# Kernel optimization log

Measured on AMD Instinct MI355X. Metric: run time of the kernel, lower is better.

The kernel has to match this reference:

```python
import jax, jax.numpy as jnp
import numpy as np

B, H, S, D = 1, 16, 4096, 64

def setup_inputs() -> dict:
    key = jax.random.key(0)
    kq, kk, kv = jax.random.split(key, 3)
    q = jax.random.normal(kq, (B, H, S, D), dtype=jnp.float32)
    k = jax.random.normal(kk, (B, H, S, D), dtype=jnp.float32)
    v = jax.random.normal(kv, (B, H, S, D), dtype=jnp.float32)
    return {"q": q, "k": k, "v": v}

def reference(q, k, v):
    # attn = q @ k^T  -> [B,H,S,S]; output = attn @ v -> [B,H,S,D]
    attn = jnp.einsum('bhqd,bhkd->bhqk', q, k)
    out = jnp.einsum('bhqk,bhkd->bhqd', attn, v)
    return out
```

## Files before the change

kernel.cpp:

```cpp
#include <hip/hip_runtime.h>
#include <stddef.h>


#define SLEN 4096
#define DIM  64
#define NH   16
#define CH   32
#define RPC  128

typedef float f4v __attribute__((ext_vector_type(4)));

__global__ __launch_bounds__(256) void kvT_partial(const float* __restrict__ K,
                                                   const float* __restrict__ V,
                                                   float* __restrict__ P) {
    const int c = blockIdx.x, h = blockIdx.y, t = threadIdx.x;
    const int wave = t >> 6, lane = t & 63;
    const int i = lane >> 3, j = lane & 7;

    __shared__ float Ks[64][64];
    __shared__ float Vs[64][64];

    const f4v* K4 = (const f4v*)(K + ((size_t)h * SLEN + (size_t)c * RPC) * DIM);
    const f4v* V4 = (const f4v*)(V + ((size_t)h * SLEN + (size_t)c * RPC) * DIM);

    float acc[8][8];
    #pragma unroll
    for (int a = 0; a < 8; ++a) {
        #pragma unroll
        for (int b = 0; b < 8; ++b) acc[a][b] = 0.f;
    }

    f4v kst[4], vst[4];
    #pragma unroll
    for (int u = 0; u < 4; ++u) { kst[u] = K4[u * 256 + t]; vst[u] = V4[u * 256 + t]; }

    for (int tile = 0; tile < 2; ++tile) {
        __syncthreads();
        #pragma unroll
        for (int u = 0; u < 4; ++u) {
            int idx = u * 256 + t, row = idx >> 4, c4 = idx & 15;
            *(f4v*)&Ks[row][c4 * 4] = kst[u];
            *(f4v*)&Vs[row][c4 * 4] = vst[u];
        }
        __syncthreads();
        if (tile == 0) {
            #pragma unroll
            for (int u = 0; u < 4; ++u) {
                kst[u] = K4[1024 + u * 256 + t];
                vst[u] = V4[1024 + u * 256 + t];
            }
        }
        #pragma unroll
        for (int s0 = 0; s0 < 16; ++s0) {
            const int s = wave * 16 + s0;
            float kf[8], vf[8];
            *(f4v*)&kf[0] = *(const f4v*)&Ks[s][i * 8];
            *(f4v*)&kf[4] = *(const f4v*)&Ks[s][i * 8 + 4];
            *(f4v*)&vf[0] = *(const f4v*)&Vs[s][j * 8];
            *(f4v*)&vf[4] = *(const f4v*)&Vs[s][j * 8 + 4];
            #pragma unroll
            for (int a = 0; a < 8; ++a) {
                #pragma unroll
                for (int b = 0; b < 8; ++b)
                    acc[a][b] = fmaf(kf[a], vf[b], acc[a][b]);
            }
        }
    }

    __syncthreads();
    float* M0 = &Ks[0][0];
    float* M1 = &Vs[0][0];
    if (wave == 0 || wave == 2) {
        float* dst = (wave == 0) ? M0 : M1;
        #pragma unroll
        for (int r = 0; r < 8; ++r) {
            #pragma unroll
            for (int hh = 0; hh < 2; ++hh) {
                f4v x; x[0]=acc[r][hh*4]; x[1]=acc[r][hh*4+1]; x[2]=acc[r][hh*4+2]; x[3]=acc[r][hh*4+3];
                *(f4v*)&dst[(i * 8 + r) * 64 + j * 8 + hh * 4] = x;
            }
        }
    }
    __syncthreads();
    if (wave == 1 || wave == 3) {
        float* dst = (wave == 1) ? M0 : M1;
        #pragma unroll
        for (int r = 0; r < 8; ++r) {
            #pragma unroll
            for (int hh = 0; hh < 2; ++hh) {
                f4v x = *(f4v*)&dst[(i * 8 + r) * 64 + j * 8 + hh * 4];
                x[0]+=acc[r][hh*4]; x[1]+=acc[r][hh*4+1]; x[2]+=acc[r][hh*4+2]; x[3]+=acc[r][hh*4+3];
                *(f4v*)&dst[(i * 8 + r) * 64 + j * 8 + hh * 4] = x;
            }
        }
    }
    __syncthreads();
    float* Pc = P + ((size_t)h * CH + c) * (DIM * DIM);
    #pragma unroll
    for (int u = 0; u < 4; ++u) {
        int idx = u * 256 + t;
        f4v x = ((const f4v*)M0)[idx] + ((const f4v*)M1)[idx];
        ((f4v*)Pc)[idx] = x;
    }
}

__global__ __launch_bounds__(256) void reduceM(const float* __restrict__ P,
                                               float* __restrict__ M) {
    const int q = blockIdx.x, h = blockIdx.y, t = threadIdx.x;
    const int off = q * 256 + t;
    const f4v* Ph = (const f4v*)(P + (size_t)h * CH * DIM * DIM);
    f4v sum; sum[0]=0.f; sum[1]=0.f; sum[2]=0.f; sum[3]=0.f;
    #pragma unroll
    for (int c = 0; c < CH; ++c) sum += Ph[(size_t)c * (DIM * DIM / 4) + off];
    ((f4v*)(M + (size_t)h * DIM * DIM))[off] = sum;
}

__global__ __launch_bounds__(64) void qm_kernel(const float* __restrict__ Q,
                                                const float* __restrict__ Mm,
                                                float* __restrict__ O) {
    const int chunk = blockIdx.x, h = blockIdx.y, lane = threadIdx.x;
    const int i = lane >> 3, j = lane & 7;

    __shared__ float Qs[64][64];
    __shared__ float Ms[64][64];

    const f4v* Q4 = (const f4v*)(Q + ((size_t)h * SLEN + (size_t)chunk * 64) * DIM);
    const f4v* M4 = (const f4v*)(Mm + (size_t)h * DIM * DIM);

    #pragma unroll
    for (int u = 0; u < 16; ++u) {
        int idx = u * 64 + lane, row = idx >> 4, c4 = idx & 15;
        int c4s = c4 ^ (row >> 3);
        *(f4v*)&Qs[row][c4s * 4] = Q4[idx];
        *(f4v*)&Ms[row][c4 * 4]  = M4[idx];
    }
    __syncthreads();

    float acc[8][8];
    #pragma unroll
    for (int a = 0; a < 8; ++a) {
        #pragma unroll
        for (int b = 0; b < 8; ++b) acc[a][b] = 0.f;
    }

    #pragma unroll
    for (int d0 = 0; d0 < DIM; d0 += 4) {
        const int c4q = d0 >> 2;
        float qf[8][4];
        #pragma unroll
        for (int r = 0; r < 8; ++r)
            *(f4v*)&qf[r][0] = *(const f4v*)&Qs[i * 8 + r][(c4q ^ i) * 4];
        float mf[4][8];
        #pragma unroll
        for (int cc = 0; cc < 4; ++cc) {
            *(f4v*)&mf[cc][0] = *(const f4v*)&Ms[d0 + cc][j * 8];
            *(f4v*)&mf[cc][4] = *(const f4v*)&Ms[d0 + cc][j * 8 + 4];
        }
        #pragma unroll
        for (int r = 0; r < 8; ++r) {
            #pragma unroll
            for (int cc = 0; cc < 4; ++cc) {
                #pragma unroll
                for (int b = 0; b < 8; ++b)
                    acc[r][b] = fmaf(qf[r][cc], mf[cc][b], acc[r][b]);
            }
        }
    }

    float* Orow = O + ((size_t)h * SLEN + (size_t)chunk * 64) * DIM;
    #pragma unroll
    for (int r = 0; r < 8; ++r) {
        #pragma unroll
        for (int hh = 0; hh < 2; ++hh) {
            f4v x; x[0]=acc[r][hh*4]; x[1]=acc[r][hh*4+1]; x[2]=acc[r][hh*4+2]; x[3]=acc[r][hh*4+3];
            *(f4v*)&Orow[(i * 8 + r) * DIM + j * 8 + hh * 4] = x;
        }
    }
}

extern "C" void kernel_launch(void* const* d_in, const int* in_sizes, int n_in,
                              void* d_out, int out_size, void* d_ws, size_t ws_size,
                              hipStream_t stream) {
    const float* q = (const float*)d_in[0];
    const float* k = (const float*)d_in[1];
    const float* v = (const float*)d_in[2];
    float* out = (float*)d_out;
    float* P = (float*)d_ws;
    float* M = P + (size_t)NH * CH * DIM * DIM;

    kvT_partial<<<dim3(CH, NH), 256, 0, stream>>>(k, v, P);
    reduceM<<<dim3(4, NH), 256, 0, stream>>>(P, M);
    qm_kernel<<<dim3(SLEN / 64, NH), 64, 0, stream>>>(q, M, out);
}
```

Measured before the change: 111.6 us.

## Rewrite Q·M kernel with 256 threads, 4x4 tiles and direct global loads

The final Q@(K^T V) kernel goes from one 64-thread wave computing 8x8 output tiles out of LDS-staged Q and M to 256 threads, each computing a 4x4 tile. Operands are read straight from global memory (relying on cache), with no shared memory and no barrier. This raises parallelism per block and occupancy and removes the LDS staging and its sync. In exchange, each thread does more global loads per FMA and the redundant Q/M reads depend on cache hits.

```diff
diff --git a/kernel.cpp b/kernel.cpp
--- a/kernel.cpp
+++ b/kernel.cpp
@@ -115,66 +115,42 @@
     ((f4v*)(M + (size_t)h * DIM * DIM))[off] = sum;
 }
 
-__global__ __launch_bounds__(64) void qm_kernel(const float* __restrict__ Q,
-                                                const float* __restrict__ Mm,
-                                                float* __restrict__ O) {
-    const int chunk = blockIdx.x, h = blockIdx.y, lane = threadIdx.x;
-    const int i = lane >> 3, j = lane & 7;
+__global__ __launch_bounds__(256) void qm_kernel(const float* __restrict__ Q,
+                                                 const float* __restrict__ Mm,
+                                                 float* __restrict__ O) {
+    const int chunk = blockIdx.x, h = blockIdx.y, t = threadIdx.x;
+    const int i = t >> 4, j = t & 15;
 
-    __shared__ float Qs[64][64];
-    __shared__ float Ms[64][64];
-
-    const f4v* Q4 = (const f4v*)(Q + ((size_t)h * SLEN + (size_t)chunk * 64) * DIM);
+    const f4v* Q4 = (const f4v*)(Q + ((size_t)h * SLEN + (size_t)chunk * 64 + i * 4) * DIM);
     const f4v* M4 = (const f4v*)(Mm + (size_t)h * DIM * DIM);
 
-    #pragma unroll
-    for (int u = 0; u < 16; ++u) {
-        int idx = u * 64 + lane, row = idx >> 4, c4 = idx & 15;
-        int c4s = c4 ^ (row >> 3);
-        *(f4v*)&Qs[row][c4s * 4] = Q4[idx];
-        *(f4v*)&Ms[row][c4 * 4]  = M4[idx];
-    }
-    __syncthreads();
+    float acc[4][4] = {{0.f,0.f,0.f,0.f},{0.f,0.f,0.f,0.f},
+                       {0.f,0.f,0.f,0.f},{0.f,0.f,0.f,0.f}};
 
-    float acc[8][8];
-    #pragma unroll
-    for (int a = 0; a < 8; ++a) {
+    #pragma unroll 4
+    for (int d0 = 0; d0 < 16; ++d0) {
+        f4v qf[4], mf[4];
         #pragma unroll
-        for (int b = 0; b < 8; ++b) acc[a][b] = 0.f;
+        for (int a = 0; a < 4; ++a)
+            qf[a] = Q4[a * 16 + d0];
+        #pragma unroll
+        for (int cc = 0; cc < 4; ++cc)
+            mf[cc] = M4[(d0 * 4 + cc) * 16 + j];
+        #pragma unroll
+        for (int a = 0; a < 4; ++a)
+            #pragma unroll
+            for (int cc = 0; cc < 4; ++cc)
+                #pragma unroll
+                for (int b = 0; b < 4; ++b)
+                    acc[a][b] = fmaf(qf[a][cc], mf[cc][b], acc[a][b]);
     }
 
+    f4v* O4 = (f4v*)(O + ((size_t)h * SLEN + (size_t)chunk * 64 + i * 4) * DIM);
     #pragma unroll
-    for (int d0 = 0; d0 < DIM; d0 += 4) {
-        const int c4q = d0 >> 2;
-        float qf[8][4];
-        #pragma unroll
-        for (int r = 0; r < 8; ++r)
-            *(f4v*)&qf[r][0] = *(const f4v*)&Qs[i * 8 + r][(c4q ^ i) * 4];
-        float mf[4][8];
-        #pragma unroll
-        for (int cc = 0; cc < 4; ++cc) {
-            *(f4v*)&mf[cc][0] = *(const f4v*)&Ms[d0 + cc][j * 8];
-            *(f4v*)&mf[cc][4] = *(const f4v*)&Ms[d0 + cc][j * 8 + 4];
-        }
-        #pragma unroll
-        for (int r = 0; r < 8; ++r) {
-            #pragma unroll
-            for (int cc = 0; cc < 4; ++cc) {
-                #pragma unroll
-                for (int b = 0; b < 8; ++b)
-                    acc[r][b] = fmaf(qf[r][cc], mf[cc][b], acc[r][b]);
-            }
-        }
-    }
-
-    float* Orow = O + ((size_t)h * SLEN + (size_t)chunk * 64) * DIM;
-    #pragma unroll
-    for (int r = 0; r < 8; ++r) {
-        #pragma unroll
-        for (int hh = 0; hh < 2; ++hh) {
-            f4v x; x[0]=acc[r][hh*4]; x[1]=acc[r][hh*4+1]; x[2]=acc[r][hh*4+2]; x[3]=acc[r][hh*4+3];
-            *(f4v*)&Orow[(i * 8 + r) * DIM + j * 8 + hh * 4] = x;
-        }
+    for (int a = 0; a < 4; ++a) {
+        f4v res;
+        res[0] = acc[a][0]; res[1] = acc[a][1]; res[2] = acc[a][2]; res[3] = acc[a][3];
+        O4[a * 16 + j] = res;
     }
 }
 
@@ -190,5 +166,5 @@
 
     kvT_partial<<<dim3(CH, NH), 256, 0, stream>>>(k, v, P);
     reduceM<<<dim3(4, NH), 256, 0, stream>>>(P, M);
-    qm_kernel<<<dim3(SLEN / 64, NH), 64, 0, stream>>>(q, M, out);
+    qm_kernel<<<dim3(SLEN / 64, NH), 256, 0, stream>>>(q, M, out);
 }
```

After: 118.3 us. +6.1%, slower.
